# Performance work log

Hardware: AMD Instinct MI355X
Metric: run time of the kernel (lower is better)

The kernel has to match this reference:

```python
import jax, jax.numpy as jnp
import numpy as np

ACT_BITS = 8
GROUP = 64
EPS = 1e-8


def absmax_quantize_dequant(x, bits=ACT_BITS, group_size=GROUP):
    """Group-wise (per-token) absmax fake-quantize to signed `bits` ints, then dequantize.
    Straight-through estimator: gradient flows as identity through the quantizer."""
    qmax = 2 ** (bits - 1) - 1  # 127 for 8 bits
    orig_shape = x.shape
    xg = x.reshape(*orig_shape[:-1], orig_shape[-1] // group_size, group_size)
    scale = jnp.maximum(jnp.max(jnp.abs(xg), axis=-1, keepdims=True), EPS)
    q = jnp.clip(jnp.round(xg / scale * qmax), -qmax, qmax)
    xq = (q * scale / qmax).reshape(orig_shape)
    # STE: forward = xq, backward = identity
    return x + jax.lax.stop_gradient(xq - x)


def binary_weight_quantize_centered(W):
    """Per-row centered binarization: sign(W - mean) scaled by per-row mean |.| (BitNet 1-bit).
    Straight-through estimator on the weights."""
    Wc = W - jnp.mean(W, axis=1, keepdims=True)          # [out, in]
    alpha = jnp.mean(jnp.abs(Wc), axis=1, keepdims=True)  # per-row scale [out, 1]
    Wb = jnp.sign(Wc) * alpha
    return W + jax.lax.stop_gradient(Wb - W)


def setup_inputs() -> dict:
    key = jax.random.key(0)
    kx, kw = jax.random.split(key)
    B, S, D_IN, D_OUT = 4, 2048, 4096, 4096
    x = jax.random.normal(kx, (B, S, D_IN), dtype=jnp.float32)
    # kaiming-uniform-ish init scale
    bound = float(np.sqrt(1.0 / D_IN))
    W = jax.random.uniform(kw, (D_OUT, D_IN), dtype=jnp.float32, minval=-bound, maxval=bound)
    return {"x": x, "W": W}


def reference(x, W):
    x_q = absmax_quantize_dequant(x)
    Wb = binary_weight_quantize_centered(W)
    # F.linear(x_q, Wb): y[b,s,o] = sum_d x_q[b,s,d] * Wb[o,d]
    return jnp.einsum('bsd,od->bso', x_q, Wb)
```

## Files before the change

### kernel.cpp

```cpp
#include <hip/hip_runtime.h>
#include <hip/hip_bf16.h>
#include <stdint.h>
#include <stddef.h>

typedef _Float16 f16;
typedef _Float16 f16x4 __attribute__((ext_vector_type(4)));
typedef _Float16 f16x8 __attribute__((ext_vector_type(8)));
typedef float    f32x4 __attribute__((ext_vector_type(4)));

__device__ __forceinline__ void gload16(const void* g, void* l) {
  __builtin_amdgcn_global_load_lds(
      (__attribute__((address_space(1))) void*)g,
      (__attribute__((address_space(3))) void*)l,
      16, 0, 0);
}

__device__ __forceinline__ void BAR() {
  asm volatile("" ::: "memory");
  __builtin_amdgcn_s_barrier();
  asm volatile("" ::: "memory");
}

__global__ __launch_bounds__(256) void prep_w_kernel(
    const float* __restrict__ W, f16* __restrict__ sgn,
    float* __restrict__ alpha, int K)
{
  const int row = blockIdx.x;
  const int tid = threadIdx.x;
  const float4* Wr = (const float4*)(W + (size_t)row * K);

  float4 v[4];
#pragma unroll
  for (int j = 0; j < 4; ++j) v[j] = Wr[j * 256 + tid];

  __shared__ float red1[4];
  __shared__ float red2[4];

  float s = 0.f;
#pragma unroll
  for (int j = 0; j < 4; ++j) s += (v[j].x + v[j].y) + (v[j].z + v[j].w);
#pragma unroll
  for (int m = 32; m >= 1; m >>= 1) s += __shfl_xor(s, m);
  if ((tid & 63) == 0) red1[tid >> 6] = s;
  __syncthreads();
  const float mean = (red1[0] + red1[1] + red1[2] + red1[3]) * (1.0f / 4096.0f);

  float a = 0.f;
#pragma unroll
  for (int j = 0; j < 4; ++j) {
    a += fabsf(v[j].x - mean) + fabsf(v[j].y - mean) +
         fabsf(v[j].z - mean) + fabsf(v[j].w - mean);
  }
#pragma unroll
  for (int m = 32; m >= 1; m >>= 1) a += __shfl_xor(a, m);
  if ((tid & 63) == 0) red2[tid >> 6] = a;

  f16x4* so = (f16x4*)(sgn + (size_t)row * K);
#pragma unroll
  for (int j = 0; j < 4; ++j) {
    float w0 = v[j].x - mean, w1 = v[j].y - mean,
          w2 = v[j].z - mean, w3 = v[j].w - mean;
    f16x4 o;
    o[0] = (f16)((w0 > 0.f) ? 1.f : ((w0 < 0.f) ? -1.f : 0.f));
    o[1] = (f16)((w1 > 0.f) ? 1.f : ((w1 < 0.f) ? -1.f : 0.f));
    o[2] = (f16)((w2 > 0.f) ? 1.f : ((w2 < 0.f) ? -1.f : 0.f));
    o[3] = (f16)((w3 > 0.f) ? 1.f : ((w3 < 0.f) ? -1.f : 0.f));
    so[j * 256 + tid] = o;
  }
  __syncthreads();
  if (tid == 0)
    alpha[row] = (red2[0] + red2[1] + red2[2] + red2[3]) * (1.0f / 4096.0f);
}

__global__ __launch_bounds__(256) void quant_x_kernel(
    const float4* __restrict__ x4, f16x4* __restrict__ xq4)
{
  const int i = blockIdx.x * 256 + threadIdx.x;
  float4 v = x4[i];
  float am = fmaxf(fmaxf(fabsf(v.x), fabsf(v.y)),
                   fmaxf(fabsf(v.z), fabsf(v.w)));
  am = fmaxf(am, __shfl_xor(am, 1));
  am = fmaxf(am, __shfl_xor(am, 2));
  am = fmaxf(am, __shfl_xor(am, 4));
  am = fmaxf(am, __shfl_xor(am, 8));
  const float scale = fmaxf(am, 1e-8f);

  float q0 = fminf(fmaxf(rintf(v.x / scale * 127.0f), -127.0f), 127.0f);
  float q1 = fminf(fmaxf(rintf(v.y / scale * 127.0f), -127.0f), 127.0f);
  float q2 = fminf(fmaxf(rintf(v.z / scale * 127.0f), -127.0f), 127.0f);
  float q3 = fminf(fmaxf(rintf(v.w / scale * 127.0f), -127.0f), 127.0f);

  f16x4 o;
  o[0] = (f16)(q0 * scale / 127.0f);
  o[1] = (f16)(q1 * scale / 127.0f);
  o[2] = (f16)(q2 * scale / 127.0f);
  o[3] = (f16)(q3 * scale / 127.0f);
  xq4[i] = o;
}

#define BM 256
#define BN 256
#define BK 64

__global__ __launch_bounds__(512, 2) void gemm_kernel(
    const f16* __restrict__ A,
    const f16* __restrict__ Bt,
    const float* __restrict__ alpha,
    float* __restrict__ C, int M, int N, int K)
{
  __shared__ __align__(16) char smem[131072];

  const int tid  = threadIdx.x;
  const int wave = tid >> 6;
  const int lane = tid & 63;
  const int wm = wave >> 2;
  const int wn = wave & 3;

  const int nbx = N / BN;
  const int nwg = gridDim.x;
  const int cpx = nwg >> 3;
  const int bid = blockIdx.x;
  const int swz = (bid & 7) * cpx + (bid >> 3);
  const int bn = (swz % nbx) * BN;
  const int bm = (swz / nbx) * BM;

  const int lrow = lane & 15;
  const int lk   = (lane >> 4) * 8;
  const int rxor = (lrow & 7) << 4;
  const int colx = (lk * 2) ^ rxor;
  const int aob  = wm * 16384 + lrow * 128 + colx;
  const int bob  = 32768 + (wn >> 1) * 16384 + ((wn & 1) * 64 + lrow) * 128 + colx;

  const int srow = lane >> 3;
  const int ksrc = ((lane & 7) ^ srow) * 8;
  const size_t lsoff = (size_t)srow * K + ksrc;

#define RDA(BUF, mi, kh) (*(const f16x8*)(smem + (BUF) + (aob ^ ((kh)*64)) + (mi)*2048))
#define RDB(BUF, ni, kh) (*(const f16x8*)(smem + (BUF) + (bob ^ ((kh)*64)) + (ni)*2048))

#define STAGE(LDSOFF, MAT, GROW, T) do {                                        \
    const f16* _s = (MAT) + (size_t)((GROW) + wave * 8) * K + (size_t)(T) * 64; \
    gload16(_s + lsoff, smem + (LDSOFF) + wave * 1024);                         \
    gload16(_s + (size_t)64 * K + lsoff, smem + (LDSOFF) + 8192 + wave * 1024); \
  } while (0)

#define MMQ(AARR, BARR, MBASE) do {                                             \
    _Pragma("unroll")                                                           \
    for (int mi = 0; mi < 4; ++mi) {                                            \
      _Pragma("unroll")                                                         \
      for (int ni = 0; ni < 4; ++ni) {                                          \
        acc[(MBASE) + mi][ni] = __builtin_amdgcn_mfma_f32_16x16x32_f16(         \
            AARR[(MBASE) + mi], BARR[ni], acc[(MBASE) + mi][ni], 0, 0, 0);      \
      }                                                                         \
    }                                                                           \
  } while (0)

  f32x4 acc[8][4] = {};
  f16x8 a0[8], a1[8], bq0[4], bq1[4];

  const int nk = K / BK;

  STAGE(0,             A,  bm,       0);
  STAGE(16384,         A,  bm + 128, 0);
  STAGE(32768,         Bt, bn,       0);
  STAGE(49152,         Bt, bn + 128, 0);
  STAGE(65536 + 32768, Bt, bn,      1);
  asm volatile("s_waitcnt vmcnt(2)" ::: "memory");
  BAR();

  for (int it = 0; it < nk / 2; ++it) {
    const int t1 = 2 * it + 1;
    int t2 = 2 * it + 2; if (t2 >= nk) t2 -= nk;
    int t3 = 2 * it + 3; if (t3 >= nk) t3 -= nk;

#pragma unroll
    for (int mi = 0; mi < 4; ++mi) a0[mi] = RDA(0, mi, 0);
#pragma unroll
    for (int ni = 0; ni < 4; ++ni) bq0[ni] = RDB(0, ni, 0);
#pragma unroll
    for (int mi = 4; mi < 8; ++mi) a0[mi] = RDA(0, mi, 0);
    STAGE(65536 + 49152, Bt, bn + 128, t1);
    BAR();
    __builtin_amdgcn_s_setprio(1);
    MMQ(a0, bq0, 0);
    __builtin_amdgcn_s_setprio(0);
    BAR();

#pragma unroll
    for (int mi = 0; mi < 4; ++mi) a1[mi] = RDA(0, mi, 1);
#pragma unroll
    for (int ni = 0; ni < 4; ++ni) bq1[ni] = RDB(0, ni, 1);
    STAGE(65536, A, bm, t1);
    BAR();
    __builtin_amdgcn_s_setprio(1);
    MMQ(a0, bq0, 4);
    __builtin_amdgcn_s_setprio(0);
    BAR();

#pragma unroll
    for (int mi = 4; mi < 8; ++mi) a1[mi] = RDA(0, mi, 1);
    STAGE(65536 + 16384, A, bm + 128, t1);
    BAR();
    __builtin_amdgcn_s_setprio(1);
    MMQ(a1, bq1, 0);
    __builtin_amdgcn_s_setprio(0);
    BAR();

    STAGE(32768, Bt, bn, t2);
    asm volatile("s_waitcnt vmcnt(2)" ::: "memory");
    BAR();
    __builtin_amdgcn_s_setprio(1);
    MMQ(a1, bq1, 4);
    __builtin_amdgcn_s_setprio(0);
    BAR();

#pragma unroll
    for (int mi = 0; mi < 4; ++mi) a0[mi] = RDA(65536, mi, 0);
#pragma unroll
    for (int ni = 0; ni < 4; ++ni) bq0[ni] = RDB(65536, ni, 0);
#pragma unroll
    for (int mi = 4; mi < 8; ++mi) a0[mi] = RDA(65536, mi, 0);
    STAGE(49152, Bt, bn + 128, t2);
    BAR();
    __builtin_amdgcn_s_setprio(1);
    MMQ(a0, bq0, 0);
    __builtin_amdgcn_s_setprio(0);
    BAR();

#pragma unroll
    for (int mi = 0; mi < 4; ++mi) a1[mi] = RDA(65536, mi, 1);
#pragma unroll
    for (int ni = 0; ni < 4; ++ni) bq1[ni] = RDB(65536, ni, 1);
    STAGE(0, A, bm, t2);
    BAR();
    __builtin_amdgcn_s_setprio(1);
    MMQ(a0, bq0, 4);
    __builtin_amdgcn_s_setprio(0);
    BAR();

#pragma unroll
    for (int mi = 4; mi < 8; ++mi) a1[mi] = RDA(65536, mi, 1);
    STAGE(16384, A, bm + 128, t2);
    BAR();
    __builtin_amdgcn_s_setprio(1);
    MMQ(a1, bq1, 0);
    __builtin_amdgcn_s_setprio(0);
    BAR();

    STAGE(65536 + 32768, Bt, bn, t3);
    asm volatile("s_waitcnt vmcnt(2)" ::: "memory");
    BAR();
    __builtin_amdgcn_s_setprio(1);
    MMQ(a1, bq1, 4);
    __builtin_amdgcn_s_setprio(0);
    BAR();
  }

  const int r0 = bm + wm * 128 + ((lane >> 4) << 2);
  const int c0 = bn + wn * 64 + (lane & 15);
#pragma unroll
  for (int ni = 0; ni < 4; ++ni) {
    const int n = c0 + ni * 16;
    const float alv = alpha[n];
#pragma unroll
    for (int mi = 0; mi < 8; ++mi) {
#pragma unroll
      for (int r = 0; r < 4; ++r) {
        C[(size_t)(r0 + mi * 16 + r) * N + n] = acc[mi][ni][r] * alv;
      }
    }
  }
}

extern "C" void kernel_launch(void* const* d_in, const int* in_sizes, int n_in,
                              void* d_out, int out_size, void* d_ws, size_t ws_size,
                              hipStream_t stream) {
  const float* x = (const float*)d_in[0];
  const float* W = (const float*)d_in[1];
  float* y = (float*)d_out;

  const int K = 4096;
  const int M = in_sizes[0] / K;
  const int N = in_sizes[1] / K;

  f16*   xq    = (f16*)d_ws;
  f16*   sgn   = (f16*)((char*)d_ws + (size_t)M * K * 2);
  float* alpha = (float*)((char*)d_ws + (size_t)M * K * 2 + (size_t)N * K * 2);

  prep_w_kernel<<<N, 256, 0, stream>>>(W, sgn, alpha, K);

  const int n4 = (M * K) / 4;
  quant_x_kernel<<<n4 / 256, 256, 0, stream>>>((const float4*)x, (f16x4*)xq);

  const int nblk = (M / BM) * (N / BN);
  gemm_kernel<<<nblk, 512, 0, stream>>>(xq, sgn, alpha, y, M, N, K);
}
```

Before: 495.7 us.

## Restructure GEMM main loop into one-barrier-per-tile double-buffered pipeline

Replaces the eight-phase unrolled main loop, which had many barriers and split fragment loads, with a simpler loop that uses one barrier per K tile. Each step loads the next k-half fragments from LDS while the MFMAs for the current fragments run. After the barrier it loads the following tile's fragments and issues global-to-LDS staging for tile t+2 into the freed buffer. The aim is to cut barrier and synchronisation overhead and give longer MFMA runs, at the cost of waiting on vmcnt(0) every tile and holding more fragment registers live.

```diff
diff --git a/kernel.cpp b/kernel.cpp
--- a/kernel.cpp
+++ b/kernel.cpp
@@ -13,12 +13,6 @@
       (__attribute__((address_space(1))) void*)g,
       (__attribute__((address_space(3))) void*)l,
       16, 0, 0);
-}
-
-__device__ __forceinline__ void BAR() {
-  asm volatile("" ::: "memory");
-  __builtin_amdgcn_s_barrier();
-  asm volatile("" ::: "memory");
 }
 
 __global__ __launch_bounds__(256) void prep_w_kernel(
@@ -144,117 +138,81 @@
     gload16(_s + (size_t)64 * K + lsoff, smem + (LDSOFF) + 8192 + wave * 1024); \
   } while (0)
 
-#define MMQ(AARR, BARR, MBASE) do {                                             \
+#define STAGE_TILE(BUF, T) do {                                                 \
+    STAGE((BUF) +     0, A,  bm,       (T));                                    \
+    STAGE((BUF) + 16384, A,  bm + 128, (T));                                    \
+    STAGE((BUF) + 32768, Bt, bn,       (T));                                    \
+    STAGE((BUF) + 49152, Bt, bn + 128, (T));                                    \
+  } while (0)
+
+#define MM32(AF, BF) do {                                                       \
     _Pragma("unroll")                                                           \
-    for (int mi = 0; mi < 4; ++mi) {                                            \
+    for (int mi = 0; mi < 8; ++mi) {                                            \
       _Pragma("unroll")                                                         \
       for (int ni = 0; ni < 4; ++ni) {                                          \
-        acc[(MBASE) + mi][ni] = __builtin_amdgcn_mfma_f32_16x16x32_f16(         \
-            AARR[(MBASE) + mi], BARR[ni], acc[(MBASE) + mi][ni], 0, 0, 0);      \
+        acc[mi][ni] = __builtin_amdgcn_mfma_f32_16x16x32_f16(                   \
+            AF[mi], BF[ni], acc[mi][ni], 0, 0, 0);                              \
       }                                                                         \
     }                                                                           \
   } while (0)
 
   f32x4 acc[8][4] = {};
-  f16x8 a0[8], a1[8], bq0[4], bq1[4];
+  f16x8 fcA[8], fcB[4], fnA[8], fnB[4];
 
   const int nk = K / BK;
 
-  STAGE(0,             A,  bm,       0);
-  STAGE(16384,         A,  bm + 128, 0);
-  STAGE(32768,         Bt, bn,       0);
-  STAGE(49152,         Bt, bn + 128, 0);
-  STAGE(65536 + 32768, Bt, bn,      1);
-  asm volatile("s_waitcnt vmcnt(2)" ::: "memory");
-  BAR();
-
-  for (int it = 0; it < nk / 2; ++it) {
-    const int t1 = 2 * it + 1;
-    int t2 = 2 * it + 2; if (t2 >= nk) t2 -= nk;
-    int t3 = 2 * it + 3; if (t3 >= nk) t3 -= nk;
-
-#pragma unroll
-    for (int mi = 0; mi < 4; ++mi) a0[mi] = RDA(0, mi, 0);
-#pragma unroll
-    for (int ni = 0; ni < 4; ++ni) bq0[ni] = RDB(0, ni, 0);
-#pragma unroll
-    for (int mi = 4; mi < 8; ++mi) a0[mi] = RDA(0, mi, 0);
-    STAGE(65536 + 49152, Bt, bn + 128, t1);
-    BAR();
+  STAGE_TILE(0, 0);
+  STAGE_TILE(65536, 1);
+  asm volatile("s_waitcnt vmcnt(8)" ::: "memory");
+  __builtin_amdgcn_sched_barrier(0);
+  __builtin_amdgcn_s_barrier();
+  asm volatile("" ::: "memory");
+
+#pragma unroll
+  for (int mi = 0; mi < 8; ++mi) fcA[mi] = RDA(0, mi, 0);
+#pragma unroll
+  for (int ni = 0; ni < 4; ++ni) fcB[ni] = RDB(0, ni, 0);
+
+  for (int t = 0; t < nk - 1; ++t) {
+    const int b  = (t & 1) ? 65536 : 0;
+    const int nb = 65536 - b;
+
+#pragma unroll
+    for (int mi = 0; mi < 8; ++mi) fnA[mi] = RDA(b, mi, 1);
+#pragma unroll
+    for (int ni = 0; ni < 4; ++ni) fnB[ni] = RDB(b, ni, 1);
+
     __builtin_amdgcn_s_setprio(1);
-    MMQ(a0, bq0, 0);
+    MM32(fcA, fcB);
     __builtin_amdgcn_s_setprio(0);
-    BAR();
-
-#pragma unroll
-    for (int mi = 0; mi < 4; ++mi) a1[mi] = RDA(0, mi, 1);
-#pragma unroll
-    for (int ni = 0; ni < 4; ++ni) bq1[ni] = RDB(0, ni, 1);
-    STAGE(65536, A, bm, t1);
-    BAR();
+
+    asm volatile("s_waitcnt lgkmcnt(0)" ::: "memory");
+    asm volatile("s_waitcnt vmcnt(0)" ::: "memory");
+    __builtin_amdgcn_sched_barrier(0);
+    __builtin_amdgcn_s_barrier();
+    asm volatile("" ::: "memory");
+
+#pragma unroll
+    for (int mi = 0; mi < 8; ++mi) fcA[mi] = RDA(nb, mi, 0);
+#pragma unroll
+    for (int ni = 0; ni < 4; ++ni) fcB[ni] = RDB(nb, ni, 0);
+
+    int t2 = t + 2; if (t2 >= nk) t2 -= nk;
+    STAGE_TILE(b, t2);
+
     __builtin_amdgcn_s_setprio(1);
-    MMQ(a0, bq0, 4);
+    MM32(fnA, fnB);
     __builtin_amdgcn_s_setprio(0);
-    BAR();
-
-#pragma unroll
-    for (int mi = 4; mi < 8; ++mi) a1[mi] = RDA(0, mi, 1);
-    STAGE(65536 + 16384, A, bm + 128, t1);
-    BAR();
-    __builtin_amdgcn_s_setprio(1);
-    MMQ(a1, bq1, 0);
-    __builtin_amdgcn_s_setprio(0);
-    BAR();
-
-    STAGE(32768, Bt, bn, t2);
-    asm volatile("s_waitcnt vmcnt(2)" ::: "memory");
-    BAR();
-    __builtin_amdgcn_s_setprio(1);
-    MMQ(a1, bq1, 4);
-    __builtin_amdgcn_s_setprio(0);
-    BAR();
-
-#pragma unroll
-    for (int mi = 0; mi < 4; ++mi) a0[mi] = RDA(65536, mi, 0);
-#pragma unroll
-    for (int ni = 0; ni < 4; ++ni) bq0[ni] = RDB(65536, ni, 0);
-#pragma unroll
-    for (int mi = 4; mi < 8; ++mi) a0[mi] = RDA(65536, mi, 0);
-    STAGE(49152, Bt, bn + 128, t2);
-    BAR();
-    __builtin_amdgcn_s_setprio(1);
-    MMQ(a0, bq0, 0);
-    __builtin_amdgcn_s_setprio(0);
-    BAR();
-
-#pragma unroll
-    for (int mi = 0; mi < 4; ++mi) a1[mi] = RDA(65536, mi, 1);
-#pragma unroll
-    for (int ni = 0; ni < 4; ++ni) bq1[ni] = RDB(65536, ni, 1);
-    STAGE(0, A, bm, t2);
-    BAR();
-    __builtin_amdgcn_s_setprio(1);
-    MMQ(a0, bq0, 4);
-    __builtin_amdgcn_s_setprio(0);
-    BAR();
-
-#pragma unroll
-    for (int mi = 4; mi < 8; ++mi) a1[mi] = RDA(65536, mi, 1);
-    STAGE(16384, A, bm + 128, t2);
-    BAR();
-    __builtin_amdgcn_s_setprio(1);
-    MMQ(a1, bq1, 0);
-    __builtin_amdgcn_s_setprio(0);
-    BAR();
-
-    STAGE(65536 + 32768, Bt, bn, t3);
-    asm volatile("s_waitcnt vmcnt(2)" ::: "memory");
-    BAR();
-    __builtin_amdgcn_s_setprio(1);
-    MMQ(a1, bq1, 4);
-    __builtin_amdgcn_s_setprio(0);
-    BAR();
-  }
+  }
+
+#pragma unroll
+  for (int mi = 0; mi < 8; ++mi) fnA[mi] = RDA(65536, mi, 1);
+#pragma unroll
+  for (int ni = 0; ni < 4; ++ni) fnB[ni] = RDB(65536, ni, 1);
+  __builtin_amdgcn_s_setprio(1);
+  MM32(fcA, fcB);
+  MM32(fnA, fnB);
+  __builtin_amdgcn_s_setprio(0);
 
   const int r0 = bm + wm * 128 + ((lane >> 4) << 2);
   const int c0 = bn + wn * 64 + (lane & 15);
```

Result: faster. 473.7 us (-4.4%).
